# Optimization experiments

Hardware: AMD Instinct MI355X
Metric: run time of the kernel (lower is better)

## Reference

```python
import jax, jax.numpy as jnp
import numpy as np


def setup_inputs() -> dict:
    key = jax.random.key(0)
    k1, k2, k3, k4 = jax.random.split(key, 4)
    B, D, C, N = 8192, 2048, 2048, 8
    x = jax.random.normal(k1, (B, D), dtype=jnp.float32)
    W = jax.random.normal(k2, (N, C, D), dtype=jnp.float32) * (1.0 / np.sqrt(D))
    b = jax.random.normal(k3, (N, C), dtype=jnp.float32) * 0.02
    factor = jnp.full((N,), 1.0 / N, dtype=jnp.float32)
    return {"x": x, "W": W, "b": b, "factor": factor}


def reference(x, W, b, factor):
    # Per-head linear: heads[b, n, c] = x @ W[n].T + b[n]
    heads = jnp.einsum("bd,ncd->bnc", x, W) + b[None, :, :]
    # Weighted sum over heads with canonical_factor (torch: cat(...,-1) @ factor)
    out = jnp.einsum("bnc,n->bc", heads, factor)
    return out
```

## Files before the change

kernel.cpp:

```cpp
#include <hip/hip_runtime.h>


#define MDIM 8192
#define KDIM 2048
#define NDIM 2048
#define NHEADS 8

#define BM 128
#define BN 128
#define BK 64

using bf16x8 = __attribute__((ext_vector_type(8))) short;
using f32x4  = __attribute__((ext_vector_type(4))) float;

__device__ __forceinline__ unsigned short f2bf(float x) {
    unsigned int u = __float_as_uint(x);
    u += 0x7FFFu + ((u >> 16) & 1u);
    return (unsigned short)(u >> 16);
}

__device__ __forceinline__ void async_load16(const void* g, void* l) {
    __builtin_amdgcn_global_load_lds(
        (const __attribute__((address_space(1))) unsigned int*)g,
        (__attribute__((address_space(3))) unsigned int*)l,
        16, 0, 0);
}

__global__ __launch_bounds__(256) void prep_kernel(
    const float* __restrict__ x,
    const float* __restrict__ W,
    const float* __restrict__ b,
    const float* __restrict__ factor,
    unsigned short* __restrict__ xbf,
    unsigned short* __restrict__ Wbf,
    float* __restrict__ beff) {
    const int gtid = blockIdx.x * 256 + threadIdx.x;

    {
        size_t base = (size_t)gtid * 16;
        float4 v0 = *reinterpret_cast<const float4*>(x + base);
        float4 v1 = *reinterpret_cast<const float4*>(x + base + 4);
        float4 v2 = *reinterpret_cast<const float4*>(x + base + 8);
        float4 v3 = *reinterpret_cast<const float4*>(x + base + 12);
        union { unsigned short u[16]; uint4 q[2]; } o;
        o.u[0]  = f2bf(v0.x); o.u[1]  = f2bf(v0.y); o.u[2]  = f2bf(v0.z); o.u[3]  = f2bf(v0.w);
        o.u[4]  = f2bf(v1.x); o.u[5]  = f2bf(v1.y); o.u[6]  = f2bf(v1.z); o.u[7]  = f2bf(v1.w);
        o.u[8]  = f2bf(v2.x); o.u[9]  = f2bf(v2.y); o.u[10] = f2bf(v2.z); o.u[11] = f2bf(v2.w);
        o.u[12] = f2bf(v3.x); o.u[13] = f2bf(v3.y); o.u[14] = f2bf(v3.z); o.u[15] = f2bf(v3.w);
        *reinterpret_cast<uint4*>(xbf + base)     = o.q[0];
        *reinterpret_cast<uint4*>(xbf + base + 8) = o.q[1];
    }

    if (gtid < 524288) {
        const size_t CD = (size_t)NDIM * KDIM;
        size_t base = (size_t)gtid * 8;
        float f[NHEADS];
#pragma unroll
        for (int n = 0; n < NHEADS; ++n) f[n] = factor[n];
        float a0 = 0.f, a1 = 0.f, a2 = 0.f, a3 = 0.f;
        float a4 = 0.f, a5 = 0.f, a6 = 0.f, a7 = 0.f;
#pragma unroll
        for (int n = 0; n < NHEADS; ++n) {
            float4 lo = *reinterpret_cast<const float4*>(W + (size_t)n * CD + base);
            float4 hi = *reinterpret_cast<const float4*>(W + (size_t)n * CD + base + 4);
            a0 += f[n] * lo.x; a1 += f[n] * lo.y; a2 += f[n] * lo.z; a3 += f[n] * lo.w;
            a4 += f[n] * hi.x; a5 += f[n] * hi.y; a6 += f[n] * hi.z; a7 += f[n] * hi.w;
        }
        union { unsigned short u[8]; uint4 q; } o;
        o.u[0] = f2bf(a0); o.u[1] = f2bf(a1); o.u[2] = f2bf(a2); o.u[3] = f2bf(a3);
        o.u[4] = f2bf(a4); o.u[5] = f2bf(a5); o.u[6] = f2bf(a6); o.u[7] = f2bf(a7);
        *reinterpret_cast<uint4*>(Wbf + base) = o.q;
    }

    if (gtid < NDIM) {
        float s = 0.f;
#pragma unroll
        for (int n = 0; n < NHEADS; ++n) s += factor[n] * b[(size_t)n * NDIM + gtid];
        beff[gtid] = s;
    }
}

__global__ __launch_bounds__(256) void gemm_bt_kernel(
    const unsigned short* __restrict__ A,
    const unsigned short* __restrict__ B,
    const float* __restrict__ bias,
    float* __restrict__ C)
{
    __shared__ unsigned short As[BM * BK];
    __shared__ unsigned short Bs[BN * BK];

    const int tid  = threadIdx.x;
    const int lane = tid & 63;
    const int w    = tid >> 6;
    const int m16  = lane & 15;
    const int quad = lane >> 4;

    const int bid = blockIdx.x;
    const int g   = bid >> 3;
    const int nt  = (bid & 7) * 2 + (g & 1);
    const int mt  = g >> 1;
    const int blockN0 = nt * BN;
    const int blockM0 = mt * BM;

    const int wr = (w >> 1) * 64;
    const int wc = (w & 1) * 64;

    const int srow = lane >> 3;
    const int scol = ((lane & 7) ^ srow) * 8;
    const unsigned short* aP[4];
    const unsigned short* bP[4];
    unsigned short* aL[4];
    unsigned short* bL[4];
#pragma unroll
    for (int i = 0; i < 4; ++i) {
        int r = i * 32 + w * 8;
        aP[i] = A + (size_t)(blockM0 + r + srow) * KDIM + scol;
        bP[i] = B + (size_t)(blockN0 + r + srow) * KDIM + scol;
        aL[i] = As + (size_t)r * BK;
        bL[i] = Bs + (size_t)r * BK;
    }

    f32x4 acc[4][4] = {};

    for (int k0 = 0; k0 < KDIM; k0 += BK) {
#pragma unroll
        for (int i = 0; i < 4; ++i) {
            async_load16(aP[i], aL[i]);
            async_load16(bP[i], bL[i]);
            aP[i] += BK; bP[i] += BK;
        }
        __syncthreads();

#pragma unroll
        for (int kk = 0; kk < BK; kk += 32) {
            bf16x8 af[4], bfr[4];
#pragma unroll
            for (int rt = 0; rt < 4; ++rt) {
                int row = wr + rt * 16 + m16;
                int gA = ((kk >> 3) + quad) ^ (row & 7);
                af[rt] = *reinterpret_cast<const bf16x8*>(&As[(size_t)row * BK + gA * 8]);
            }
#pragma unroll
            for (int ct = 0; ct < 4; ++ct) {
                int row = wc + ct * 16 + m16;
                int gB = ((kk >> 3) + quad) ^ (row & 7);
                bfr[ct] = *reinterpret_cast<const bf16x8*>(&Bs[(size_t)row * BK + gB * 8]);
            }
#pragma unroll
            for (int rt = 0; rt < 4; ++rt)
#pragma unroll
                for (int ct = 0; ct < 4; ++ct)
                    acc[rt][ct] = __builtin_amdgcn_mfma_f32_16x16x32_bf16(
                        af[rt], bfr[ct], acc[rt][ct], 0, 0, 0);
        }
        __syncthreads();
    }

    float bv[4];
#pragma unroll
    for (int ct = 0; ct < 4; ++ct) bv[ct] = bias[blockN0 + wc + ct * 16 + m16];
#pragma unroll
    for (int rt = 0; rt < 4; ++rt) {
        int row0 = blockM0 + wr + rt * 16 + quad * 4;
#pragma unroll
        for (int ct = 0; ct < 4; ++ct) {
            int col = blockN0 + wc + ct * 16 + m16;
#pragma unroll
            for (int r = 0; r < 4; ++r)
                C[(size_t)(row0 + r) * NDIM + col] = acc[rt][ct][r] + bv[ct];
        }
    }
}

extern "C" void kernel_launch(void* const* d_in, const int* in_sizes, int n_in,
                              void* d_out, int out_size, void* d_ws, size_t ws_size,
                              hipStream_t stream) {
    const float* x      = (const float*)d_in[0];
    const float* W      = (const float*)d_in[1];
    const float* b      = (const float*)d_in[2];
    const float* factor = (const float*)d_in[3];
    float* out = (float*)d_out;

    unsigned short* xbf  = (unsigned short*)d_ws;
    unsigned short* Wbf  = (unsigned short*)((char*)d_ws + 33554432);
    float*          beff = (float*)((char*)d_ws + 33554432 + 8388608);

    prep_kernel<<<dim3(4096), dim3(256), 0, stream>>>(x, W, b, factor, xbf, Wbf, beff);
    gemm_bt_kernel<<<dim3(1024), dim3(256), 0, stream>>>(xbf, Wbf, beff, out);
}
```

Measured before the change: 332.0 us.

## Fuse x fp32-to-bf16 conversion into GEMM A-tile load, drop x prepass

The separate pass that converted x to bf16 is removed. The GEMM now streams fp32 x tiles straight into LDS with an XOR swizzle and packs them to bf16 by truncation while building MFMA fragments. This saves writing and re-reading the 32MB bf16 copy of x. In exchange the A-tile LDS footprint doubles and each K step moves twice as many A bytes, which could lower occupancy and raise per-tile load traffic. Truncation also replaces round-to-nearest for x. The prep kernel now only reduces W, and its loads are hoisted ahead of the accumulation for more memory-level parallelism.

```diff
diff --git a/kernel.cpp b/kernel.cpp
--- a/kernel.cpp
+++ b/kernel.cpp
@@ -19,6 +19,11 @@
     return (unsigned short)(u >> 16);
 }
 
+__device__ __forceinline__ unsigned int pk_trunc(float hi, float lo) {
+    return __builtin_amdgcn_perm(__float_as_uint(hi), __float_as_uint(lo),
+                                 0x07060302u);
+}
+
 __device__ __forceinline__ void async_load16(const void* g, void* l) {
     __builtin_amdgcn_global_load_lds(
         (const __attribute__((address_space(1))) unsigned int*)g,
@@ -27,50 +32,39 @@
 }
 
 __global__ __launch_bounds__(256) void prep_kernel(
-    const float* __restrict__ x,
     const float* __restrict__ W,
     const float* __restrict__ b,
     const float* __restrict__ factor,
-    unsigned short* __restrict__ xbf,
     unsigned short* __restrict__ Wbf,
     float* __restrict__ beff) {
     const int gtid = blockIdx.x * 256 + threadIdx.x;
+    const size_t CD = (size_t)NDIM * KDIM;
+    const size_t base = (size_t)gtid * 8;
 
-    {
-        size_t base = (size_t)gtid * 16;
-        float4 v0 = *reinterpret_cast<const float4*>(x + base);
-        float4 v1 = *reinterpret_cast<const float4*>(x + base + 4);
-        float4 v2 = *reinterpret_cast<const float4*>(x + base + 8);
-        float4 v3 = *reinterpret_cast<const float4*>(x + base + 12);
-        union { unsigned short u[16]; uint4 q[2]; } o;
-        o.u[0]  = f2bf(v0.x); o.u[1]  = f2bf(v0.y); o.u[2]  = f2bf(v0.z); o.u[3]  = f2bf(v0.w);
-        o.u[4]  = f2bf(v1.x); o.u[5]  = f2bf(v1.y); o.u[6]  = f2bf(v1.z); o.u[7]  = f2bf(v1.w);
-        o.u[8]  = f2bf(v2.x); o.u[9]  = f2bf(v2.y); o.u[10] = f2bf(v2.z); o.u[11] = f2bf(v2.w);
-        o.u[12] = f2bf(v3.x); o.u[13] = f2bf(v3.y); o.u[14] = f2bf(v3.z); o.u[15] = f2bf(v3.w);
-        *reinterpret_cast<uint4*>(xbf + base)     = o.q[0];
-        *reinterpret_cast<uint4*>(xbf + base + 8) = o.q[1];
+    float f[NHEADS];
+#pragma unroll
+    for (int n = 0; n < NHEADS; ++n) f[n] = factor[n];
+
+    float4 L[16];
+#pragma unroll
+    for (int n = 0; n < NHEADS; ++n) {
+        L[2 * n]     = *reinterpret_cast<const float4*>(W + (size_t)n * CD + base);
+        L[2 * n + 1] = *reinterpret_cast<const float4*>(W + (size_t)n * CD + base + 4);
     }
 
-    if (gtid < 524288) {
-        const size_t CD = (size_t)NDIM * KDIM;
-        size_t base = (size_t)gtid * 8;
-        float f[NHEADS];
+    float a0 = 0.f, a1 = 0.f, a2 = 0.f, a3 = 0.f;
+    float a4 = 0.f, a5 = 0.f, a6 = 0.f, a7 = 0.f;
 #pragma unroll
-        for (int n = 0; n < NHEADS; ++n) f[n] = factor[n];
-        float a0 = 0.f, a1 = 0.f, a2 = 0.f, a3 = 0.f;
-        float a4 = 0.f, a5 = 0.f, a6 = 0.f, a7 = 0.f;
-#pragma unroll
-        for (int n = 0; n < NHEADS; ++n) {
-            float4 lo = *reinterpret_cast<const float4*>(W + (size_t)n * CD + base);
-            float4 hi = *reinterpret_cast<const float4*>(W + (size_t)n * CD + base + 4);
-            a0 += f[n] * lo.x; a1 += f[n] * lo.y; a2 += f[n] * lo.z; a3 += f[n] * lo.w;
-            a4 += f[n] * hi.x; a5 += f[n] * hi.y; a6 += f[n] * hi.z; a7 += f[n] * hi.w;
-        }
-        union { unsigned short u[8]; uint4 q; } o;
-        o.u[0] = f2bf(a0); o.u[1] = f2bf(a1); o.u[2] = f2bf(a2); o.u[3] = f2bf(a3);
-        o.u[4] = f2bf(a4); o.u[5] = f2bf(a5); o.u[6] = f2bf(a6); o.u[7] = f2bf(a7);
-        *reinterpret_cast<uint4*>(Wbf + base) = o.q;
+    for (int n = 0; n < NHEADS; ++n) {
+        a0 += f[n] * L[2 * n].x;     a1 += f[n] * L[2 * n].y;
+        a2 += f[n] * L[2 * n].z;     a3 += f[n] * L[2 * n].w;
+        a4 += f[n] * L[2 * n + 1].x; a5 += f[n] * L[2 * n + 1].y;
+        a6 += f[n] * L[2 * n + 1].z; a7 += f[n] * L[2 * n + 1].w;
     }
+    union { unsigned short u[8]; uint4 q; } o;
+    o.u[0] = f2bf(a0); o.u[1] = f2bf(a1); o.u[2] = f2bf(a2); o.u[3] = f2bf(a3);
+    o.u[4] = f2bf(a4); o.u[5] = f2bf(a5); o.u[6] = f2bf(a6); o.u[7] = f2bf(a7);
+    *reinterpret_cast<uint4*>(Wbf + base) = o.q;
 
     if (gtid < NDIM) {
         float s = 0.f;
@@ -81,12 +75,12 @@
 }
 
 __global__ __launch_bounds__(256) void gemm_bt_kernel(
-    const unsigned short* __restrict__ A,
+    const float* __restrict__ A,
     const unsigned short* __restrict__ B,
     const float* __restrict__ bias,
     float* __restrict__ C)
 {
-    __shared__ unsigned short As[BM * BK];
+    __shared__ float          As[BM * BK];
     __shared__ unsigned short Bs[BN * BK];
 
     const int tid  = threadIdx.x;
@@ -105,18 +99,27 @@
     const int wr = (w >> 1) * 64;
     const int wc = (w & 1) * 64;
 
-    const int srow = lane >> 3;
-    const int scol = ((lane & 7) ^ srow) * 8;
-    const unsigned short* aP[4];
+    const int sArow = lane >> 4;
+    const int sAgr  = lane & 15;
+    const int rmodA = w * 4 + sArow;
+    const int gcolA = (sAgr ^ rmodA) * 4;
+    const float* aP[8];
+    float* aL[8];
+#pragma unroll
+    for (int i = 0; i < 8; ++i) {
+        int r = i * 16 + w * 4;
+        aP[i] = A + (size_t)(blockM0 + r + sArow) * KDIM + gcolA;
+        aL[i] = As + (size_t)r * BK;
+    }
+
+    const int sBrow = lane >> 3;
+    const int sBcol = ((lane & 7) ^ sBrow) * 8;
     const unsigned short* bP[4];
-    unsigned short* aL[4];
     unsigned short* bL[4];
 #pragma unroll
     for (int i = 0; i < 4; ++i) {
         int r = i * 32 + w * 8;
-        aP[i] = A + (size_t)(blockM0 + r + srow) * KDIM + scol;
-        bP[i] = B + (size_t)(blockN0 + r + srow) * KDIM + scol;
-        aL[i] = As + (size_t)r * BK;
+        bP[i] = B + (size_t)(blockN0 + r + sBrow) * KDIM + sBcol;
         bL[i] = Bs + (size_t)r * BK;
     }
 
@@ -124,11 +127,9 @@
 
     for (int k0 = 0; k0 < KDIM; k0 += BK) {
 #pragma unroll
-        for (int i = 0; i < 4; ++i) {
-            async_load16(aP[i], aL[i]);
-            async_load16(bP[i], bL[i]);
-            aP[i] += BK; bP[i] += BK;
-        }
+        for (int i = 0; i < 8; ++i) { async_load16(aP[i], aL[i]); aP[i] += BK; }
+#pragma unroll
+        for (int i = 0; i < 4; ++i) { async_load16(bP[i], bL[i]); bP[i] += BK; }
         __syncthreads();
 
 #pragma unroll
@@ -137,8 +138,17 @@
 #pragma unroll
             for (int rt = 0; rt < 4; ++rt) {
                 int row = wr + rt * 16 + m16;
-                int gA = ((kk >> 3) + quad) ^ (row & 7);
-                af[rt] = *reinterpret_cast<const bf16x8*>(&As[(size_t)row * BK + gA * 8]);
+                int g0  = (kk >> 2) + quad * 2;
+                const float4 lo = *reinterpret_cast<const float4*>(
+                    &As[(size_t)row * BK + ((g0)     ^ m16) * 4]);
+                const float4 hi = *reinterpret_cast<const float4*>(
+                    &As[(size_t)row * BK + ((g0 + 1) ^ m16) * 4]);
+                union { bf16x8 v; unsigned int u[4]; } t;
+                t.u[0] = pk_trunc(lo.y, lo.x);
+                t.u[1] = pk_trunc(lo.w, lo.z);
+                t.u[2] = pk_trunc(hi.y, hi.x);
+                t.u[3] = pk_trunc(hi.w, hi.z);
+                af[rt] = t.v;
             }
 #pragma unroll
             for (int ct = 0; ct < 4; ++ct) {
@@ -181,10 +191,9 @@
     const float* factor = (const float*)d_in[3];
     float* out = (float*)d_out;
 
-    unsigned short* xbf  = (unsigned short*)d_ws;
-    unsigned short* Wbf  = (unsigned short*)((char*)d_ws + 33554432);
-    float*          beff = (float*)((char*)d_ws + 33554432 + 8388608);
+    unsigned short* Wbf  = (unsigned short*)d_ws;
+    float*          beff = (float*)((char*)d_ws + 8388608);
 
-    prep_kernel<<<dim3(4096), dim3(256), 0, stream>>>(x, W, b, factor, xbf, Wbf, beff);
-    gemm_bt_kernel<<<dim3(1024), dim3(256), 0, stream>>>(xbf, Wbf, beff, out);
+    prep_kernel<<<dim3(2048), dim3(256), 0, stream>>>(W, b, factor, Wbf, beff);
+    gemm_bt_kernel<<<dim3(1024), dim3(256), 0, stream>>>(x, Wbf, beff, out);
 }
```

Measured after the change: 351.3 us. 5.8% more time.
